# Performance work log

Measured on AMD Instinct MI355X. Metric: run time of the kernel, lower is better.

## Reference

```python
import jax, jax.numpy as jnp
import numpy as np

# (top, left, bottom, right) box layout, per module constants
B, T, R, C = 32, 200, 4096, 81
REDUCTION = 16.0
IOU_THRESH = 0.7


def _make_boxes(key, b, n):
    k1, k2 = jax.random.split(key)
    cyx = jax.random.uniform(k1, (b, n, 2), minval=100.0, maxval=700.0)
    hw = jax.random.uniform(k2, (b, n, 2), minval=48.0, maxval=256.0)
    top = cyx[..., 0] - hw[..., 0] * 0.5
    left = cyx[..., 1] - hw[..., 1] * 0.5
    bottom = cyx[..., 0] + hw[..., 0] * 0.5
    right = cyx[..., 1] + hw[..., 1] * 0.5
    return jnp.stack([top, left, bottom, right], axis=-1)


def setup_inputs() -> dict:
    key = jax.random.key(0)
    ks = jax.random.split(key, 6)
    nms_reg = _make_boxes(ks[0], B, R)                              # [B,R,4] proposal boxes
    # ground-truth boxes: jittered copies of the first T proposals so many IoUs exceed 0.7
    bboxes = nms_reg[:, :T, :] + jax.random.normal(ks[1], (B, T, 4)) * 4.0
    classes = jax.random.randint(ks[2], (B, T), 0, C)               # [B,T] int labels
    rcnn_reg = jax.random.normal(ks[3], (B, R, 4)) * 0.1            # predicted box deltas
    rcnn_cls = jax.random.normal(ks[4], (B, R, C))                  # class logits
    nms_cls = jax.random.normal(ks[5], (B, R, 2))                   # unused by forward
    return {"nms_reg": nms_reg, "nms_cls": nms_cls, "rcnn_reg": rcnn_reg,
            "rcnn_cls": rcnn_cls, "bboxes": bboxes, "classes": classes}


def _iou(a, b):
    # a, b broadcastable [..., 4] in (top,left,bottom,right)
    t = jnp.maximum(a[..., 0], b[..., 0])
    l = jnp.maximum(a[..., 1], b[..., 1])
    bb = jnp.minimum(a[..., 2], b[..., 2])
    r = jnp.minimum(a[..., 3], b[..., 3])
    inter = jnp.clip(bb - t, 0.0) * jnp.clip(r - l, 0.0)
    area_a = (a[..., 2] - a[..., 0]) * (a[..., 3] - a[..., 1])
    area_b = (b[..., 2] - b[..., 0]) * (b[..., 3] - b[..., 1])
    return inter / (area_a + area_b - inter)


def reference(nms_reg, nms_cls, rcnn_reg, rcnn_cls, bboxes, classes):
    dt = rcnn_reg.dtype
    # pairwise IoU between proposals and GT boxes: [B, T, R]
    iou = _iou(nms_reg[:, None, :, :], bboxes[:, :, None, :])
    # torch sorts along T and takes the last slice == argmax over targets.
    # (gathers of rcnn_reg / rcnn_cls along T are identities since they are
    #  constant along T, so max_reg == rcnn_reg, max_rcnn_cls == rcnn_cls.)
    best = jnp.argmax(iou, axis=1)                                  # [B,R]
    max_iou = jnp.max(iou, axis=1)                                  # [B,R]
    max_bboxes = jnp.take_along_axis(bboxes, best[:, :, None], axis=1)   # [B,R,4]
    max_classes = jnp.take_along_axis(classes, best, axis=1)             # [B,R]

    mask = (max_iou > IOU_THRESH).astype(dt)                        # [B,R]
    npos = jnp.sum(mask)
    denom = jnp.maximum(npos, 1.0)

    # CrossEntropy over positives (mean reduction over masked elements)
    logp = jax.nn.log_softmax(rcnn_cls, axis=-1)
    ce = -jnp.take_along_axis(logp, max_classes[..., None], axis=-1)[..., 0]
    cls_loss = jnp.sum(ce * mask) / denom

    # categorical accuracy over positives
    acc = jnp.sum((jnp.argmax(rcnn_cls, axis=-1) == max_classes).astype(dt) * mask) / denom

    # normalized by rounded height/width
    rounded = jnp.round(max_bboxes / REDUCTION) * REDUCTION
    h = rounded[..., 2] - rounded[..., 0]
    w = rounded[..., 3] - rounded[..., 1]
    h = jnp.where(h == 0, 1.0, h)
    w = jnp.where(w == 0, 1.0, w)
    off = max_bboxes - rounded
    tgt = jnp.stack([off[..., 0] / h, off[..., 1] / w,
                     off[..., 2] / h, off[..., 3] / w], axis=-1)    # [B,R,4]

    d = jnp.abs(rcnn_reg - tgt)
    sl1 = jnp.where(d < 1.0, 0.5 * d * d, d - 0.5)
    # torch applies SmoothL1 (mean over positives) per coordinate, then sums
    reg_loss = jnp.sum(jnp.sum(sl1 * mask[..., None], axis=(0, 1)) / denom)

    has_pos = npos > 0
    z = jnp.zeros((), dt)
    return (jnp.where(has_pos, cls_loss, z),
            jnp.where(has_pos, reg_loss, z),
            jnp.where(has_pos, acc, z))
```

## Files before the change

### kernel.cpp

```cpp
#include <hip/hip_runtime.h>

#define BB 32
#define TT 200
#define RR 4096
#define CC 81
#define IOU_THRESH 0.7f
#define RED 16.0f

__global__ __launch_bounds__(256) void rcnn_main_kernel(
    const float* __restrict__ nms_reg,
    const float* __restrict__ rcnn_reg,
    const float* __restrict__ rcnn_cls,
    const float* __restrict__ bboxes,
    const int*   __restrict__ classes,
    float* __restrict__ ws)
{
    __shared__ float s_box[TT * 4];
    __shared__ int   s_cls[TT];
    __shared__ float s_red[4][4];

    const int tid = threadIdx.x;
    const int blocks_per_b = RR / 256;
    const int b = blockIdx.x / blocks_per_b;
    const int r = (blockIdx.x % blocks_per_b) * 256 + tid;

    for (int i = tid; i < TT * 4; i += 256) s_box[i] = bboxes[(long)b * TT * 4 + i];
    for (int i = tid; i < TT;     i += 256) s_cls[i] = classes[(long)b * TT + i];
    __syncthreads();

    const float4 a = *(const float4*)&nms_reg[((long)b * RR + r) * 4];
    const float area_a = (a.z - a.x) * (a.w - a.y);

    float best_iou = -1.0f;
    int   best_t   = 0;
    #pragma unroll 4
    for (int t = 0; t < TT; ++t) {
        const float gt = s_box[t * 4 + 0];
        const float gl = s_box[t * 4 + 1];
        const float gb = s_box[t * 4 + 2];
        const float gr = s_box[t * 4 + 3];
        const float it = fmaxf(a.x, gt);
        const float il = fmaxf(a.y, gl);
        const float ib = fminf(a.z, gb);
        const float ir = fminf(a.w, gr);
        const float inter = fmaxf(ib - it, 0.0f) * fmaxf(ir - il, 0.0f);
        const float area_b = (gb - gt) * (gr - gl);
        const float iou = inter / (area_a + area_b - inter);
        if (iou > best_iou) { best_iou = iou; best_t = t; }
    }

    float pos = 0.0f, ce = 0.0f, acc = 0.0f, reg = 0.0f;
    if (best_iou > IOU_THRESH) {
        pos = 1.0f;

        const float gt = s_box[best_t * 4 + 0];
        const float gl = s_box[best_t * 4 + 1];
        const float gb = s_box[best_t * 4 + 2];
        const float gr = s_box[best_t * 4 + 3];
        const float rt = rintf(gt / RED) * RED;
        const float rl = rintf(gl / RED) * RED;
        const float rb = rintf(gb / RED) * RED;
        const float rr = rintf(gr / RED) * RED;
        float h = rb - rt; if (h == 0.0f) h = 1.0f;
        float w = rr - rl; if (w == 0.0f) w = 1.0f;
        const float t0 = (gt - rt) / h;
        const float t1 = (gl - rl) / w;
        const float t2 = (gb - rb) / h;
        const float t3 = (gr - rr) / w;

        const float4 p = *(const float4*)&rcnn_reg[((long)b * RR + r) * 4];
        const float d0 = fabsf(p.x - t0);
        const float d1 = fabsf(p.y - t1);
        const float d2 = fabsf(p.z - t2);
        const float d3 = fabsf(p.w - t3);
        reg  = (d0 < 1.0f) ? 0.5f * d0 * d0 : d0 - 0.5f;
        reg += (d1 < 1.0f) ? 0.5f * d1 * d1 : d1 - 0.5f;
        reg += (d2 < 1.0f) ? 0.5f * d2 * d2 : d2 - 0.5f;
        reg += (d3 < 1.0f) ? 0.5f * d3 * d3 : d3 - 0.5f;

        const float* row = &rcnn_cls[((long)b * RR + r) * CC];
        const int cls = s_cls[best_t];
        float m = -INFINITY;
        int amax = 0;
        for (int c = 0; c < CC; ++c) {
            const float x = row[c];
            if (x > m) { m = x; amax = c; }
        }
        float s = 0.0f;
        for (int c = 0; c < CC; ++c) s += expf(row[c] - m);
        ce  = m + logf(s) - row[cls];
        acc = (amax == cls) ? 1.0f : 0.0f;
    }

    #pragma unroll
    for (int off = 32; off > 0; off >>= 1) {
        pos += __shfl_down(pos, off);
        ce  += __shfl_down(ce,  off);
        acc += __shfl_down(acc, off);
        reg += __shfl_down(reg, off);
    }
    const int wave = tid >> 6;
    const int lane = tid & 63;
    if (lane == 0) {
        s_red[wave][0] = pos;
        s_red[wave][1] = ce;
        s_red[wave][2] = acc;
        s_red[wave][3] = reg;
    }
    __syncthreads();
    if (tid == 0) {
        float P = 0.0f, E = 0.0f, A = 0.0f, G = 0.0f;
        #pragma unroll
        for (int v = 0; v < 4; ++v) {
            P += s_red[v][0];
            E += s_red[v][1];
            A += s_red[v][2];
            G += s_red[v][3];
        }
        atomicAdd(&ws[0], P);
        atomicAdd(&ws[1], E);
        atomicAdd(&ws[2], A);
        atomicAdd(&ws[3], G);
    }
}

__global__ void rcnn_final_kernel(const float* __restrict__ ws, float* __restrict__ out)
{
    const float npos  = ws[0];
    const float denom = fmaxf(npos, 1.0f);
    const bool  hp    = npos > 0.0f;
    out[0] = hp ? ws[1] / denom : 0.0f;
    out[1] = hp ? ws[3] / denom : 0.0f;
    out[2] = hp ? ws[2] / denom : 0.0f;
}

extern "C" void kernel_launch(void* const* d_in, const int* in_sizes, int n_in,
                              void* d_out, int out_size, void* d_ws, size_t ws_size,
                              hipStream_t stream) {
    const float* nms_reg  = (const float*)d_in[0];
    const float* rcnn_reg = (const float*)d_in[2];
    const float* rcnn_cls = (const float*)d_in[3];
    const float* bboxes   = (const float*)d_in[4];
    const int*   classes  = (const int*)d_in[5];
    float* ws  = (float*)d_ws;
    float* out = (float*)d_out;

    hipMemsetAsync(ws, 0, 4 * sizeof(float), stream);
    rcnn_main_kernel<<<BB * (RR / 256), 256, 0, stream>>>(
        nms_reg, rcnn_reg, rcnn_cls, bboxes, classes, ws);
    rcnn_final_kernel<<<1, 1, 0, stream>>>(ws, out);
}
```

Measured before the change: 137.9 us.

## Split IoU target scan across two threads per proposal and fuse finalize

```diff
diff --git a/kernel.cpp b/kernel.cpp
--- a/kernel.cpp
+++ b/kernel.cpp
@@ -7,89 +7,112 @@
 #define IOU_THRESH 0.7f
 #define RED 16.0f
 
-__global__ __launch_bounds__(256) void rcnn_main_kernel(
+#define BLK 256
+#define PPB 128
+#define HALF_T 100
+#define NBLOCKS (BB * (RR / PPB))
+
+__global__ __launch_bounds__(BLK) void rcnn_main_kernel(
     const float* __restrict__ nms_reg,
     const float* __restrict__ rcnn_reg,
     const float* __restrict__ rcnn_cls,
     const float* __restrict__ bboxes,
     const int*   __restrict__ classes,
-    float* __restrict__ ws)
+    float* __restrict__ ws,
+    float* __restrict__ out)
 {
-    __shared__ float s_box[TT * 4];
-    __shared__ int   s_cls[TT];
-    __shared__ float s_red[4][4];
+    __shared__ float4 s_box[TT];
+    __shared__ int    s_cls[TT];
+    __shared__ float  s_c1n[PPB];
+    __shared__ float  s_c1d[PPB];
+    __shared__ int    s_c1t[PPB];
+    __shared__ float  s_red[4][4];
 
-    const int tid = threadIdx.x;
-    const int blocks_per_b = RR / 256;
-    const int b = blockIdx.x / blocks_per_b;
-    const int r = (blockIdx.x % blocks_per_b) * 256 + tid;
+    const int tid   = threadIdx.x;
+    const int blocks_per_b = RR / PPB;
+    const int b     = blockIdx.x / blocks_per_b;
+    const int p     = tid & (PPB - 1);
+    const int chunk = tid >> 7;
+    const int r     = (blockIdx.x % blocks_per_b) * PPB + p;
 
-    for (int i = tid; i < TT * 4; i += 256) s_box[i] = bboxes[(long)b * TT * 4 + i];
-    for (int i = tid; i < TT;     i += 256) s_cls[i] = classes[(long)b * TT + i];
+    const float4* gbox = (const float4*)&bboxes[(long)b * TT * 4];
+    for (int i = tid; i < TT; i += BLK) {
+        s_box[i] = gbox[i];
+        s_cls[i] = classes[b * TT + i];
+    }
     __syncthreads();
 
-    const float4 a = *(const float4*)&nms_reg[((long)b * RR + r) * 4];
+    const float4 a = ((const float4*)nms_reg)[(long)b * RR + r];
     const float area_a = (a.z - a.x) * (a.w - a.y);
 
-    float best_iou = -1.0f;
-    int   best_t   = 0;
+    float bn = -1.0f, bd = 1.0f;
+    int   bt = 0;
+    const int tbeg = chunk * HALF_T;
     #pragma unroll 4
-    for (int t = 0; t < TT; ++t) {
-        const float gt = s_box[t * 4 + 0];
-        const float gl = s_box[t * 4 + 1];
-        const float gb = s_box[t * 4 + 2];
-        const float gr = s_box[t * 4 + 3];
-        const float it = fmaxf(a.x, gt);
-        const float il = fmaxf(a.y, gl);
-        const float ib = fminf(a.z, gb);
-        const float ir = fminf(a.w, gr);
+    for (int t = tbeg; t < tbeg + HALF_T; ++t) {
+        const float4 g = s_box[t];
+        const float it = fmaxf(a.x, g.x);
+        const float il = fmaxf(a.y, g.y);
+        const float ib = fminf(a.z, g.z);
+        const float ir = fminf(a.w, g.w);
         const float inter = fmaxf(ib - it, 0.0f) * fmaxf(ir - il, 0.0f);
-        const float area_b = (gb - gt) * (gr - gl);
-        const float iou = inter / (area_a + area_b - inter);
-        if (iou > best_iou) { best_iou = iou; best_t = t; }
+        const float uni   = area_a + (g.z - g.x) * (g.w - g.y) - inter;
+        const bool better = inter * bd > bn * uni;
+        bn = better ? inter : bn;
+        bd = better ? uni   : bd;
+        bt = better ? t     : bt;
     }
 
+    if (chunk == 1) { s_c1n[p] = bn; s_c1d[p] = bd; s_c1t[p] = bt; }
+    __syncthreads();
+
     float pos = 0.0f, ce = 0.0f, acc = 0.0f, reg = 0.0f;
-    if (best_iou > IOU_THRESH) {
-        pos = 1.0f;
+    if (chunk == 0) {
+        const float n1 = s_c1n[p];
+        const float d1 = s_c1d[p];
+        const int   t1 = s_c1t[p];
+        if (n1 * bd > bn * d1) { bn = n1; bd = d1; bt = t1; }
 
-        const float gt = s_box[best_t * 4 + 0];
-        const float gl = s_box[best_t * 4 + 1];
-        const float gb = s_box[best_t * 4 + 2];
-        const float gr = s_box[best_t * 4 + 3];
-        const float rt = rintf(gt / RED) * RED;
-        const float rl = rintf(gl / RED) * RED;
-        const float rb = rintf(gb / RED) * RED;
-        const float rr = rintf(gr / RED) * RED;
-        float h = rb - rt; if (h == 0.0f) h = 1.0f;
-        float w = rr - rl; if (w == 0.0f) w = 1.0f;
-        const float t0 = (gt - rt) / h;
-        const float t1 = (gl - rl) / w;
-        const float t2 = (gb - rb) / h;
-        const float t3 = (gr - rr) / w;
+        if (bn > IOU_THRESH * bd) {
+            pos = 1.0f;
 
-        const float4 p = *(const float4*)&rcnn_reg[((long)b * RR + r) * 4];
-        const float d0 = fabsf(p.x - t0);
-        const float d1 = fabsf(p.y - t1);
-        const float d2 = fabsf(p.z - t2);
-        const float d3 = fabsf(p.w - t3);
-        reg  = (d0 < 1.0f) ? 0.5f * d0 * d0 : d0 - 0.5f;
-        reg += (d1 < 1.0f) ? 0.5f * d1 * d1 : d1 - 0.5f;
-        reg += (d2 < 1.0f) ? 0.5f * d2 * d2 : d2 - 0.5f;
-        reg += (d3 < 1.0f) ? 0.5f * d3 * d3 : d3 - 0.5f;
+            const float4 g = s_box[bt];
+            const float rt = rintf(g.x / RED) * RED;
+            const float rl = rintf(g.y / RED) * RED;
+            const float rb = rintf(g.z / RED) * RED;
+            const float rr = rintf(g.w / RED) * RED;
+            float h = rb - rt; if (h == 0.0f) h = 1.0f;
+            float w = rr - rl; if (w == 0.0f) w = 1.0f;
+            const float t0 = (g.x - rt) / h;
+            const float t1f = (g.y - rl) / w;
+            const float t2 = (g.z - rb) / h;
+            const float t3 = (g.w - rr) / w;
 
-        const float* row = &rcnn_cls[((long)b * RR + r) * CC];
-        const int cls = s_cls[best_t];
-        float m = -INFINITY;
-        int amax = 0;
-        for (int c = 0; c < CC; ++c) {
-            const float x = row[c];
-            if (x > m) { m = x; amax = c; }
+            const float4 pr = ((const float4*)rcnn_reg)[(long)b * RR + r];
+            const float d0 = fabsf(pr.x - t0);
+            const float d1f = fabsf(pr.y - t1f);
+            const float d2 = fabsf(pr.z - t2);
+            const float d3 = fabsf(pr.w - t3);
+            reg  = (d0  < 1.0f) ? 0.5f * d0  * d0  : d0  - 0.5f;
+            reg += (d1f < 1.0f) ? 0.5f * d1f * d1f : d1f - 0.5f;
+            reg += (d2  < 1.0f) ? 0.5f * d2  * d2  : d2  - 0.5f;
+            reg += (d3  < 1.0f) ? 0.5f * d3  * d3  : d3  - 0.5f;
+
+            const float* row = &rcnn_cls[((long)b * RR + r) * CC];
+            const int cls = s_cls[bt];
+            float m = -INFINITY;
+            int amax = 0;
+            #pragma unroll 9
+            for (int c = 0; c < CC; ++c) {
+                const float x = row[c];
+                if (x > m) { m = x; amax = c; }
+            }
+            float s = 0.0f;
+            #pragma unroll 9
+            for (int c = 0; c < CC; ++c) s += __expf(row[c] - m);
+            ce  = m + __logf(s) - row[cls];
+            acc = (amax == cls) ? 1.0f : 0.0f;
         }
-        float s = 0.0f;
-        for (int c = 0; c < CC; ++c) s += expf(row[c] - m);
-        ce  = m + logf(s) - row[cls];
-        acc = (amax == cls) ? 1.0f : 0.0f;
     }
 
     #pragma unroll
@@ -100,8 +123,7 @@
         reg += __shfl_down(reg, off);
     }
     const int wave = tid >> 6;
-    const int lane = tid & 63;
-    if (lane == 0) {
+    if ((tid & 63) == 0) {
         s_red[wave][0] = pos;
         s_red[wave][1] = ce;
         s_red[wave][2] = acc;
@@ -121,17 +143,21 @@
         atomicAdd(&ws[1], E);
         atomicAdd(&ws[2], A);
         atomicAdd(&ws[3], G);
+        __threadfence();
+        unsigned int* cnt = (unsigned int*)&ws[4];
+        const unsigned int old = atomicAdd(cnt, 1u);
+        if (old == (unsigned int)(gridDim.x - 1)) {
+            const float npos = atomicAdd(&ws[0], 0.0f);
+            const float sce  = atomicAdd(&ws[1], 0.0f);
+            const float sac  = atomicAdd(&ws[2], 0.0f);
+            const float srg  = atomicAdd(&ws[3], 0.0f);
+            const float denom = fmaxf(npos, 1.0f);
+            const bool  hp = npos > 0.0f;
+            out[0] = hp ? sce / denom : 0.0f;
+            out[1] = hp ? srg / denom : 0.0f;
+            out[2] = hp ? sac / denom : 0.0f;
+        }
     }
-}
-
-__global__ void rcnn_final_kernel(const float* __restrict__ ws, float* __restrict__ out)
-{
-    const float npos  = ws[0];
-    const float denom = fmaxf(npos, 1.0f);
-    const bool  hp    = npos > 0.0f;
-    out[0] = hp ? ws[1] / denom : 0.0f;
-    out[1] = hp ? ws[3] / denom : 0.0f;
-    out[2] = hp ? ws[2] / denom : 0.0f;
 }
 
 extern "C" void kernel_launch(void* const* d_in, const int* in_sizes, int n_in,
@@ -145,8 +171,7 @@
     float* ws  = (float*)d_ws;
     float* out = (float*)d_out;
 
-    hipMemsetAsync(ws, 0, 4 * sizeof(float), stream);
-    rcnn_main_kernel<<<BB * (RR / 256), 256, 0, stream>>>(
-        nms_reg, rcnn_reg, rcnn_cls, bboxes, classes, ws);
-    rcnn_final_kernel<<<1, 1, 0, stream>>>(ws, out);
+    hipMemsetAsync(ws, 0, 8 * sizeof(float), stream);
+    rcnn_main_kernel<<<NBLOCKS, BLK, 0, stream>>>(
+        nms_reg, rcnn_reg, rcnn_cls, bboxes, classes, ws, out);
 }
```

New measurement: 168.1 us. 1.22x slower.
